# Performance work log

Measured on AMD Instinct MI355X. Metric: run time of the kernel, lower is better.

Reference implementation:

```python
import jax, jax.numpy as jnp
import numpy as np

N_NODES = 262144
N_EDGES = 524288
EMB = 256
HID = 256
NODE_VOC = 50000
POS_VOC = 1000
LN_EPS = 1e-5


def layer_norm(x, g, b):
    m = jnp.mean(x, axis=-1, keepdims=True)
    v = jnp.var(x, axis=-1, keepdims=True)
    return (x - m) * jax.lax.rsqrt(v + LN_EPS) * g + b


def sage_conv(x, src, dst, Wl, bl, Wr):
    # PyG SAGEConv, aggr='add': out = lin_l(sum_{j in N(i)} x_j) + lin_r(x_i)
    agg = jax.ops.segment_sum(x[src], dst, num_segments=N_NODES)  # [N, d_in]
    return agg @ Wl.T + bl + x @ Wr.T


def setup_inputs() -> dict:
    key = jax.random.key(0)
    ks = jax.random.split(key, 16)
    s = 0.02
    node_emb = jax.random.randint(ks[0], (N_NODES,), 0, NODE_VOC)
    pos = jax.random.randint(ks[1], (N_NODES,), 0, POS_VOC)
    edge = jax.random.randint(ks[2], (2, N_EDGES), 0, N_NODES)
    node_tab = jax.random.normal(ks[3], (NODE_VOC, EMB), jnp.float32) * s
    pos_tab = jax.random.normal(ks[4], (POS_VOC, EMB), jnp.float32) * s
    pos_tab = pos_tab.at[0].set(0.0)  # padding_idx=0
    g_emb = jnp.ones((EMB,), jnp.float32)
    b_emb = jnp.zeros((EMB,), jnp.float32)
    Wl0 = jax.random.normal(ks[5], (HID, EMB), jnp.float32) * s
    bl0 = jnp.zeros((HID,), jnp.float32)
    Wr0 = jax.random.normal(ks[6], (HID, EMB), jnp.float32) * s
    g0 = jnp.ones((HID,), jnp.float32)
    b0 = jnp.zeros((HID,), jnp.float32)
    Wl1 = jax.random.normal(ks[7], (EMB, HID), jnp.float32) * s
    bl1 = jnp.zeros((EMB,), jnp.float32)
    Wr1 = jax.random.normal(ks[8], (EMB, HID), jnp.float32) * s
    g1 = jnp.ones((EMB,), jnp.float32)
    b1 = jnp.zeros((EMB,), jnp.float32)
    return {"node_emb": node_emb, "pos": pos, "edge": edge,
            "node_tab": node_tab, "pos_tab": pos_tab,
            "g_emb": g_emb, "b_emb": b_emb,
            "Wl0": Wl0, "bl0": bl0, "Wr0": Wr0, "g0": g0, "b0": b0,
            "Wl1": Wl1, "bl1": bl1, "Wr1": Wr1, "g1": g1, "b1": b1}


def reference(node_emb, pos, edge, node_tab, pos_tab, g_emb, b_emb,
              Wl0, bl0, Wr0, g0, b0, Wl1, bl1, Wr1, g1, b1):
    src, dst = edge[0], edge[1]
    # embed + scale + positional emb; dropout is identity in eval
    h = node_tab[node_emb] * jnp.sqrt(jnp.float32(EMB)) + pos_tab[pos]
    h = layer_norm(h, g_emb, b_emb)
    for (Wl, bl, Wr, g, b) in ((Wl0, bl0, Wr0, g0, b0), (Wl1, bl1, Wr1, g1, b1)):
        h_ = jax.nn.relu(sage_conv(h, src, dst, Wl, bl, Wr))
        h = layer_norm(h_ + h, g, b)
    return h
```

## Files before the change

kernel.cpp:

```cpp
#include <hip/hip_runtime.h>
#include <hip/hip_bf16.h>
#include <stdint.h>

#define N_NODES 262144
#define N_EDGES 524288
#define EMB 256
#define LN_EPS 1e-5f
#define CSR_CAP 1024

typedef unsigned short u16;
typedef unsigned int u32;
typedef __bf16 bf16_t;
typedef __bf16 bf16x8 __attribute__((ext_vector_type(8)));
typedef float f32x4 __attribute__((ext_vector_type(4)));

__device__ __forceinline__ u16 f2bf(float f) {
    u32 u = __float_as_uint(f);
    u32 r = u + 0x7fffu + ((u >> 16) & 1u);
    return (u16)(r >> 16);
}
__device__ __forceinline__ float bf2f(u16 b) { return __uint_as_float(((u32)b) << 16); }
__device__ __forceinline__ float lo16(u32 x) { return __uint_as_float(x << 16); }
__device__ __forceinline__ float hi16(u32 x) { return __uint_as_float(x & 0xffff0000u); }

__device__ __forceinline__ void async_copy16(void* lds, const void* g) {
    __builtin_amdgcn_global_load_lds(
        (const __attribute__((address_space(1))) u32*)g,
        (__attribute__((address_space(3))) u32*)lds, 16, 0, 0);
}

__global__ __launch_bounds__(256) void convert_w_kernel(
    const float* __restrict__ a, const float* __restrict__ b,
    const float* __restrict__ c, const float* __restrict__ d,
    u16* __restrict__ out)
{
    int seg = blockIdx.x >> 6;
    int blk = blockIdx.x & 63;
    const float* src = (seg == 0) ? a : (seg == 1) ? b : (seg == 2) ? c : d;
    int off = blk * 1024 + threadIdx.x * 4;
    float4 v = *(const float4*)(src + off);
    uint2 o;
    o.x = (u32)f2bf(v.x) | ((u32)f2bf(v.y) << 16);
    o.y = (u32)f2bf(v.z) | ((u32)f2bf(v.w) << 16);
    *(uint2*)(out + seg * 65536 + off) = o;
}

__global__ __launch_bounds__(256) void embed_ln_kernel(
    const int* __restrict__ node_emb, const int* __restrict__ pos,
    const float* __restrict__ node_tab, const float* __restrict__ pos_tab,
    const float* __restrict__ g_emb, const float* __restrict__ b_emb,
    u16* __restrict__ h0)
{
    const int wid = threadIdx.x >> 6, lane = threadIdx.x & 63;
    const int row = blockIdx.x * 4 + wid;
    const int idx = node_emb[row];
    const int p = pos[row];
    float4 ra = *(const float4*)(node_tab + (size_t)idx * EMB + lane * 4);
    float4 rb = *(const float4*)(pos_tab + (size_t)p * EMB + lane * 4);
    float v0 = ra.x * 16.f + rb.x;
    float v1 = ra.y * 16.f + rb.y;
    float v2 = ra.z * 16.f + rb.z;
    float v3 = ra.w * 16.f + rb.w;
    float s = v0 + v1 + v2 + v3;
    float sq = v0 * v0 + v1 * v1 + v2 * v2 + v3 * v3;
    #pragma unroll
    for (int m = 1; m < 64; m <<= 1) { s += __shfl_xor(s, m); sq += __shfl_xor(sq, m); }
    float mean = s * (1.f / 256.f);
    float var = sq * (1.f / 256.f) - mean * mean;
    float rstd = rsqrtf(var + LN_EPS);
    float4 rg = *(const float4*)(g_emb + lane * 4);
    float4 rbt = *(const float4*)(b_emb + lane * 4);
    float o0 = (v0 - mean) * rstd * rg.x + rbt.x;
    float o1 = (v1 - mean) * rstd * rg.y + rbt.y;
    float o2 = (v2 - mean) * rstd * rg.z + rbt.z;
    float o3 = (v3 - mean) * rstd * rg.w + rbt.w;
    uint2 out;
    out.x = (u32)f2bf(o0) | ((u32)f2bf(o1) << 16);
    out.y = (u32)f2bf(o2) | ((u32)f2bf(o3) << 16);
    *(uint2*)(h0 + (size_t)row * EMB + lane * 4) = out;
}

__global__ __launch_bounds__(256) void hist_kernel(const int* __restrict__ dst, int* __restrict__ deg) {
    int e = blockIdx.x * 256 + threadIdx.x;
    atomicAdd(&deg[dst[e]], 1);
}

__global__ __launch_bounds__(1024) void scan1_kernel(const int* __restrict__ deg,
                                                     int* __restrict__ incl, int* __restrict__ bsum) {
    __shared__ int tmp[1024];
    int t = threadIdx.x, g = blockIdx.x * 1024 + t;
    tmp[t] = deg[g];
    __syncthreads();
    for (int off = 1; off < 1024; off <<= 1) {
        int x = (t >= off) ? tmp[t - off] : 0;
        __syncthreads();
        tmp[t] += x;
        __syncthreads();
    }
    incl[g] = tmp[t];
    if (t == 1023) bsum[blockIdx.x] = tmp[t];
}

__global__ __launch_bounds__(256) void scan2_kernel(const int* __restrict__ bsum, int* __restrict__ boff) {
    __shared__ int tmp[256];
    int t = threadIdx.x;
    int own = bsum[t];
    tmp[t] = own;
    __syncthreads();
    for (int off = 1; off < 256; off <<= 1) {
        int x = (t >= off) ? tmp[t - off] : 0;
        __syncthreads();
        tmp[t] += x;
        __syncthreads();
    }
    boff[t] = tmp[t] - own;
}

__global__ __launch_bounds__(256) void scan3_kernel(const int* __restrict__ incl, const int* __restrict__ deg,
                                                    const int* __restrict__ boff,
                                                    int* __restrict__ rowstart, int* __restrict__ cursor) {
    int g = blockIdx.x * 256 + threadIdx.x;
    int v = incl[g] - deg[g] + boff[g >> 10];
    rowstart[g] = v;
    cursor[g] = v;
    if (g == N_NODES - 1) rowstart[N_NODES] = N_EDGES;
}

__global__ __launch_bounds__(256) void scatter_kernel(const int* __restrict__ src, const int* __restrict__ dst,
                                                      int* __restrict__ cursor, int* __restrict__ csr) {
    int e = blockIdx.x * 256 + threadIdx.x;
    int slot = atomicAdd(&cursor[dst[e]], 1);
    csr[slot] = src[e];
}

template<bool F32OUT>
__global__ __launch_bounds__(512, 4) void gemm_fused_kernel(
    const u16* __restrict__ Hin,
    const int* __restrict__ rowstart, const int* __restrict__ csr,
    const u16* __restrict__ Wl, const u16* __restrict__ Wr,
    const float* __restrict__ bias, const float* __restrict__ gam, const float* __restrict__ bet,
    u16* __restrict__ outb, float* __restrict__ outf)
{
    __shared__ alignas(16) u16 aggA[4 * 64 * 64];
    __shared__ alignas(16) u16 lB[256 * 64];
    __shared__ int ls_row[72];
    __shared__ int lcsr[CSR_CAP];
    __shared__ float s_sum[64];
    __shared__ float s_sq[64];

    const int tid = threadIdx.x;
    const int wid = tid >> 6, lane = tid & 63;
    const int quad = lane >> 4, l16 = lane & 15;
    const int wrow = wid >> 2, wcol = wid & 3;
    const int m0 = blockIdx.x * 64;
    const int lsrc = ((lane & 7) ^ (lane >> 3)) * 8;

    auto stageB = [&](int s) {
        const int k0 = s * 64;
        const u16* Bsrc = (k0 < 256) ? (Wl + k0) : (Wr + (k0 - 256));
        #pragma unroll
        for (int t = 0; t < 4; ++t) {
            int q = wid * 4 + t;
            int n = q * 8 + (lane >> 3);
            async_copy16((char*)lB + q * 1024, Bsrc + (size_t)n * EMB + lsrc);
        }
    };
    auto stageH = [&](int t) {
        int row = tid >> 3;
        int kg = (tid & 7) ^ (row & 7);
        async_copy16((char*)aggA + (t - 4) * 8192 + tid * 16,
                     Hin + (size_t)(m0 + row) * EMB + (t - 4) * 64 + kg * 8);
    };

    stageB(0);

    const int beg_all = rowstart[m0];
    const int end_all = rowstart[m0 + 64];
    const int cnt = end_all - beg_all;
    if (tid < 65) ls_row[tid] = rowstart[m0 + tid];
    const int lim = (cnt < CSR_CAP) ? cnt : CSR_CAP;
    for (int e = tid; e < lim; e += 512) lcsr[e] = csr[beg_all + e];
    asm volatile("s_waitcnt lgkmcnt(0)\n\ts_barrier" ::: "memory");

    {
        const int grp = tid >> 4, gl = tid & 15;
        #pragma unroll 1
        for (int i = 0; i < 2; ++i) {
            const int r = grp * 2 + i;
            const int beg = ls_row[r];
            const int end = ls_row[r + 1];
            float a0[16] = {}, a1[16] = {};
            int j = beg;
            for (; j + 1 < end; j += 2) {
                int sl0 = j - beg_all, sl1 = sl0 + 1;
                int s0 = (sl0 < CSR_CAP) ? lcsr[sl0] : csr[j];
                int s1 = (sl1 < CSR_CAP) ? lcsr[sl1] : csr[j + 1];
                const u16* p0 = Hin + (size_t)s0 * EMB + gl * 16;
                const u16* p1 = Hin + (size_t)s1 * EMB + gl * 16;
                uint4 q0 = *(const uint4*)p0, q2 = *(const uint4*)(p0 + 8);
                uint4 q1 = *(const uint4*)p1, q3 = *(const uint4*)(p1 + 8);
                a0[0]  += lo16(q0.x); a0[1]  += hi16(q0.x);
                a0[2]  += lo16(q0.y); a0[3]  += hi16(q0.y);
                a0[4]  += lo16(q0.z); a0[5]  += hi16(q0.z);
                a0[6]  += lo16(q0.w); a0[7]  += hi16(q0.w);
                a0[8]  += lo16(q2.x); a0[9]  += hi16(q2.x);
                a0[10] += lo16(q2.y); a0[11] += hi16(q2.y);
                a0[12] += lo16(q2.z); a0[13] += hi16(q2.z);
                a0[14] += lo16(q2.w); a0[15] += hi16(q2.w);
                a1[0]  += lo16(q1.x); a1[1]  += hi16(q1.x);
                a1[2]  += lo16(q1.y); a1[3]  += hi16(q1.y);
                a1[4]  += lo16(q1.z); a1[5]  += hi16(q1.z);
                a1[6]  += lo16(q1.w); a1[7]  += hi16(q1.w);
                a1[8]  += lo16(q3.x); a1[9]  += hi16(q3.x);
                a1[10] += lo16(q3.y); a1[11] += hi16(q3.y);
                a1[12] += lo16(q3.z); a1[13] += hi16(q3.z);
                a1[14] += lo16(q3.w); a1[15] += hi16(q3.w);
            }
            if (j < end) {
                int sl0 = j - beg_all;
                int s0 = (sl0 < CSR_CAP) ? lcsr[sl0] : csr[j];
                const u16* p0 = Hin + (size_t)s0 * EMB + gl * 16;
                uint4 q0 = *(const uint4*)p0, q2 = *(const uint4*)(p0 + 8);
                a0[0]  += lo16(q0.x); a0[1]  += hi16(q0.x);
                a0[2]  += lo16(q0.y); a0[3]  += hi16(q0.y);
                a0[4]  += lo16(q0.z); a0[5]  += hi16(q0.z);
                a0[6]  += lo16(q0.w); a0[7]  += hi16(q0.w);
                a0[8]  += lo16(q2.x); a0[9]  += hi16(q2.x);
                a0[10] += lo16(q2.y); a0[11] += hi16(q2.y);
                a0[12] += lo16(q2.z); a0[13] += hi16(q2.z);
                a0[14] += lo16(q2.w); a0[15] += hi16(q2.w);
            }
            uint4 o0, o1;
            o0.x = (u32)f2bf(a0[0]  + a1[0])  | ((u32)f2bf(a0[1]  + a1[1])  << 16);
            o0.y = (u32)f2bf(a0[2]  + a1[2])  | ((u32)f2bf(a0[3]  + a1[3])  << 16);
            o0.z = (u32)f2bf(a0[4]  + a1[4])  | ((u32)f2bf(a0[5]  + a1[5])  << 16);
            o0.w = (u32)f2bf(a0[6]  + a1[6])  | ((u32)f2bf(a0[7]  + a1[7])  << 16);
            o1.x = (u32)f2bf(a0[8]  + a1[8])  | ((u32)f2bf(a0[9]  + a1[9])  << 16);
            o1.y = (u32)f2bf(a0[10] + a1[10]) | ((u32)f2bf(a0[11] + a1[11]) << 16);
            o1.z = (u32)f2bf(a0[12] + a1[12]) | ((u32)f2bf(a0[13] + a1[13]) << 16);
            o1.w = (u32)f2bf(a0[14] + a1[14]) | ((u32)f2bf(a0[15] + a1[15]) << 16);
            int kg0 = (2 * gl) & 7;
            int cg0 = kg0 ^ (r & 7);
            int cg1 = (kg0 + 1) ^ (r & 7);
            u16* base = &aggA[(gl >> 2) * 4096 + r * 64];
            *(uint4*)(base + cg0 * 8) = o0;
            *(uint4*)(base + cg1 * 8) = o1;
        }
    }
    asm volatile("s_waitcnt lgkmcnt(0)\n\ts_barrier" ::: "memory");

    f32x4 acc[2][4] = {};
    #pragma unroll
    for (int s = 0; s < 8; ++s) {
        if (s > 0) stageB(s);
        if (s >= 1 && s <= 4) stageH(s + 3);
        if (s >= 1 && s <= 4) asm volatile("s_waitcnt vmcnt(1)\n\ts_barrier" ::: "memory");
        else                  asm volatile("s_waitcnt vmcnt(0)\n\ts_barrier" ::: "memory");

        const u16* la = aggA + (s & 3) * 4096;
        #pragma unroll
        for (int kk = 0; kk < 2; ++kk) {
            const int g = (((kk * 4 + quad) ^ (l16 & 7)) * 8);
            bf16x8 af[2], bfr[4];
            #pragma unroll
            for (int mt = 0; mt < 2; ++mt)
                af[mt] = *(const bf16x8*)&la[(wrow * 32 + mt * 16 + l16) * 64 + g];
            #pragma unroll
            for (int nt = 0; nt < 4; ++nt)
                bfr[nt] = *(const bf16x8*)&lB[(wcol * 64 + nt * 16 + l16) * 64 + g];
            #pragma unroll
            for (int mt = 0; mt < 2; ++mt)
                #pragma unroll
                for (int nt = 0; nt < 4; ++nt)
                    acc[mt][nt] = __builtin_amdgcn_mfma_f32_16x16x32_bf16(af[mt], bfr[nt], acc[mt][nt], 0, 0, 0);
        }
        asm volatile("s_waitcnt lgkmcnt(0)\n\ts_barrier" ::: "memory");
    }

    if (tid < 64) { s_sum[tid] = 0.f; s_sq[tid] = 0.f; }
    __syncthreads();

    const int cb = wcol * 64;
    float blv[4], gv[4], bv[4];
    #pragma unroll
    for (int nt = 0; nt < 4; ++nt) {
        int col = cb + nt * 16 + l16;
        blv[nt] = bias[col]; gv[nt] = gam[col]; bv[nt] = bet[col];
    }

    #pragma unroll
    for (int mt = 0; mt < 2; ++mt) {
        #pragma unroll
        for (int i = 0; i < 4; ++i) {
            int r = wrow * 32 + mt * 16 + quad * 4 + i;
            int rowg = m0 + r;
            float rs = 0.f, rq = 0.f;
            #pragma unroll
            for (int nt = 0; nt < 4; ++nt) {
                int col = cb + nt * 16 + l16;
                float v = acc[mt][nt][i] + blv[nt];
                v = fmaxf(v, 0.f);
                v += bf2f(Hin[(size_t)rowg * EMB + col]);
                acc[mt][nt][i] = v;
                rs += v; rq += v * v;
            }
            #pragma unroll
            for (int m = 1; m < 16; m <<= 1) { rs += __shfl_xor(rs, m); rq += __shfl_xor(rq, m); }
            if (l16 == 0) { atomicAdd(&s_sum[r], rs); atomicAdd(&s_sq[r], rq); }
        }
    }
    __syncthreads();

    #pragma unroll
    for (int mt = 0; mt < 2; ++mt) {
        #pragma unroll
        for (int i = 0; i < 4; ++i) {
            int r = wrow * 32 + mt * 16 + quad * 4 + i;
            int rowg = m0 + r;
            float mean = s_sum[r] * (1.f / 256.f);
            float var = s_sq[r] * (1.f / 256.f) - mean * mean;
            float rstd = rsqrtf(var + LN_EPS);
            #pragma unroll
            for (int nt = 0; nt < 4; ++nt) {
                int col = cb + nt * 16 + l16;
                float o = (acc[mt][nt][i] - mean) * rstd * gv[nt] + bv[nt];
                if (F32OUT) outf[(size_t)rowg * EMB + col] = o;
                else        outb[(size_t)rowg * EMB + col] = f2bf(o);
            }
        }
    }
}

extern "C" void kernel_launch(void* const* d_in, const int* in_sizes, int n_in,
                              void* d_out, int out_size, void* d_ws, size_t ws_size,
                              hipStream_t stream)
{
    const int* node_emb = (const int*)d_in[0];
    const int* pos      = (const int*)d_in[1];
    const int* edge     = (const int*)d_in[2];
    const float* node_tab = (const float*)d_in[3];
    const float* pos_tab  = (const float*)d_in[4];
    const float* g_emb    = (const float*)d_in[5];
    const float* b_emb    = (const float*)d_in[6];
    const float* Wl0 = (const float*)d_in[7];
    const float* bl0 = (const float*)d_in[8];
    const float* Wr0 = (const float*)d_in[9];
    const float* g0  = (const float*)d_in[10];
    const float* b0  = (const float*)d_in[11];
    const float* Wl1 = (const float*)d_in[12];
    const float* bl1 = (const float*)d_in[13];
    const float* Wr1 = (const float*)d_in[14];
    const float* g1  = (const float*)d_in[15];
    const float* b1  = (const float*)d_in[16];

    char* w = (char*)d_ws;
    auto alloc = [&](size_t bytes) { char* p = w; w += (bytes + 255) & ~(size_t)255; return p; };
    u16* h0       = (u16*)alloc((size_t)N_NODES * EMB * 2);
    u16* h1       = (u16*)alloc((size_t)N_NODES * EMB * 2);
    u16* wbf      = (u16*)alloc((size_t)4 * 65536 * 2);
    int* deg      = (int*)alloc((size_t)N_NODES * 4);
    int* incl     = (int*)alloc((size_t)N_NODES * 4);
    int* rowstart = (int*)alloc((size_t)(N_NODES + 1) * 4);
    int* cursor   = (int*)alloc((size_t)N_NODES * 4);
    int* csr      = (int*)alloc((size_t)N_EDGES * 4);
    int* bsum     = (int*)alloc(256 * 4);
    int* boff     = (int*)alloc(256 * 4);

    float* outf = (float*)d_out;

    const int* srcv = edge;
    const int* dstv = edge + N_EDGES;

    hipMemsetAsync(deg, 0, (size_t)N_NODES * 4, stream);
    convert_w_kernel<<<256, 256, 0, stream>>>(Wl0, Wr0, Wl1, Wr1, wbf);
    embed_ln_kernel<<<N_NODES / 4, 256, 0, stream>>>(node_emb, pos, node_tab, pos_tab, g_emb, b_emb, h0);
    hist_kernel<<<N_EDGES / 256, 256, 0, stream>>>(dstv, deg);
    scan1_kernel<<<N_NODES / 1024, 1024, 0, stream>>>(deg, incl, bsum);
    scan2_kernel<<<1, 256, 0, stream>>>(bsum, boff);
    scan3_kernel<<<N_NODES / 256, 256, 0, stream>>>(incl, deg, boff, rowstart, cursor);
    scatter_kernel<<<N_EDGES / 256, 256, 0, stream>>>(srcv, dstv, cursor, csr);

    gemm_fused_kernel<false><<<N_NODES / 64, 512, 0, stream>>>(
        h0, rowstart, csr, wbf, wbf + 65536, bl0, g0, b0, h1, nullptr);
    gemm_fused_kernel<true><<<N_NODES / 64, 512, 0, stream>>>(
        h1, rowstart, csr, wbf + 131072, wbf + 196608, bl1, g1, b1, nullptr, outf);
}
```

Measured before the change: 810.2 us.

## Stage weights through registers and reuse LDS-resident H tiles for residual

Weight tiles are now loaded one stage ahead into registers and written to LDS at the start of each stage, replacing async global-to-LDS copies. The node's own feature rows are staged into a new LDS buffer plus reused aggA slots, so the residual add in the epilogue reads from LDS instead of re-reading the rows from global memory. This removes redundant global reads in the epilogue and changes the pipeline schedule. It costs extra registers and 8 KB more LDS, which may reduce occupancy.

After: 778.5 us. -3.9%, faster.

```diff
diff --git a/kernel.cpp b/kernel.cpp
--- a/kernel.cpp
+++ b/kernel.cpp
@@ -142,6 +142,7 @@
     u16* __restrict__ outb, float* __restrict__ outf)
 {
     __shared__ alignas(16) u16 aggA[4 * 64 * 64];
+    __shared__ alignas(16) u16 hX[64 * 64];
     __shared__ alignas(16) u16 lB[256 * 64];
     __shared__ int ls_row[72];
     __shared__ int lcsr[CSR_CAP];
@@ -155,24 +156,34 @@
     const int m0 = blockIdx.x * 64;
     const int lsrc = ((lane & 7) ^ (lane >> 3)) * 8;
 
-    auto stageB = [&](int s) {
+    uint4 breg0, breg1, breg2, breg3;
+    auto loadB = [&](int s) {
         const int k0 = s * 64;
         const u16* Bsrc = (k0 < 256) ? (Wl + k0) : (Wr + (k0 - 256));
-        #pragma unroll
-        for (int t = 0; t < 4; ++t) {
-            int q = wid * 4 + t;
-            int n = q * 8 + (lane >> 3);
-            async_copy16((char*)lB + q * 1024, Bsrc + (size_t)n * EMB + lsrc);
-        }
+        const int n0 = (wid * 4 + 0) * 8 + (lane >> 3);
+        const int n1 = (wid * 4 + 1) * 8 + (lane >> 3);
+        const int n2 = (wid * 4 + 2) * 8 + (lane >> 3);
+        const int n3 = (wid * 4 + 3) * 8 + (lane >> 3);
+        breg0 = *(const uint4*)(Bsrc + (size_t)n0 * EMB + lsrc);
+        breg1 = *(const uint4*)(Bsrc + (size_t)n1 * EMB + lsrc);
+        breg2 = *(const uint4*)(Bsrc + (size_t)n2 * EMB + lsrc);
+        breg3 = *(const uint4*)(Bsrc + (size_t)n3 * EMB + lsrc);
     };
-    auto stageH = [&](int t) {
+    auto writeB = [&]() {
+        *(uint4*)((char*)lB + (wid * 4 + 0) * 1024 + lane * 16) = breg0;
+        *(uint4*)((char*)lB + (wid * 4 + 1) * 1024 + lane * 16) = breg1;
+        *(uint4*)((char*)lB + (wid * 4 + 2) * 1024 + lane * 16) = breg2;
+        *(uint4*)((char*)lB + (wid * 4 + 3) * 1024 + lane * 16) = breg3;
+    };
+    auto stageH = [&](int t, u16* dst) {
         int row = tid >> 3;
         int kg = (tid & 7) ^ (row & 7);
-        async_copy16((char*)aggA + (t - 4) * 8192 + tid * 16,
+        async_copy16((char*)dst + tid * 16,
                      Hin + (size_t)(m0 + row) * EMB + (t - 4) * 64 + kg * 8);
     };
 
-    stageB(0);
+    loadB(0);
+    stageH(4, hX);
 
     const int beg_all = rowstart[m0];
     const int end_all = rowstart[m0 + 64];
@@ -192,9 +203,9 @@
             float a0[16] = {}, a1[16] = {};
             int j = beg;
             for (; j + 1 < end; j += 2) {
-                int sl0 = j - beg_all, sl1 = sl0 + 1;
-                int s0 = (sl0 < CSR_CAP) ? lcsr[sl0] : csr[j];
-                int s1 = (sl1 < CSR_CAP) ? lcsr[sl1] : csr[j + 1];
+                int sl = j - beg_all;
+                int s0 = (sl < CSR_CAP) ? lcsr[sl] : csr[j];
+                int s1 = (sl + 1 < CSR_CAP) ? lcsr[sl + 1] : csr[j + 1];
                 const u16* p0 = Hin + (size_t)s0 * EMB + gl * 16;
                 const u16* p1 = Hin + (size_t)s1 * EMB + gl * 16;
                 uint4 q0 = *(const uint4*)p0, q2 = *(const uint4*)(p0 + 8);
@@ -217,8 +228,8 @@
                 a1[14] += lo16(q3.w); a1[15] += hi16(q3.w);
             }
             if (j < end) {
-                int sl0 = j - beg_all;
-                int s0 = (sl0 < CSR_CAP) ? lcsr[sl0] : csr[j];
+                int sl = j - beg_all;
+                int s0 = (sl < CSR_CAP) ? lcsr[sl] : csr[j];
                 const u16* p0 = Hin + (size_t)s0 * EMB + gl * 16;
                 uint4 q0 = *(const uint4*)p0, q2 = *(const uint4*)(p0 + 8);
                 a0[0]  += lo16(q0.x); a0[1]  += hi16(q0.x);
@@ -252,12 +263,14 @@
     f32x4 acc[2][4] = {};
     #pragma unroll
     for (int s = 0; s < 8; ++s) {
-        if (s > 0) stageB(s);
-        if (s >= 1 && s <= 4) stageH(s + 3);
-        if (s >= 1 && s <= 4) asm volatile("s_waitcnt vmcnt(1)\n\ts_barrier" ::: "memory");
-        else                  asm volatile("s_waitcnt vmcnt(0)\n\ts_barrier" ::: "memory");
-
-        const u16* la = aggA + (s & 3) * 4096;
+        if (s >= 1 && s <= 3) stageH(s + 4, aggA + (s - 1) * 4096);
+        writeB();
+        if (s < 7) loadB(s + 1);
+        asm volatile("s_waitcnt lgkmcnt(0)\n\ts_barrier" ::: "memory");
+
+        const u16* la = (s < 4) ? (aggA + s * 4096)
+                      : (s == 4) ? hX
+                                 : (aggA + (s - 5) * 4096);
         #pragma unroll
         for (int kk = 0; kk < 2; ++kk) {
             const int g = (((kk * 4 + quad) ^ (l16 & 7)) * 8);
@@ -280,6 +293,7 @@
     if (tid < 64) { s_sum[tid] = 0.f; s_sq[tid] = 0.f; }
     __syncthreads();
 
+    const u16* resbuf = (wcol == 0) ? hX : (aggA + (wcol - 1) * 4096);
     const int cb = wcol * 64;
     float blv[4], gv[4], bv[4];
     #pragma unroll
@@ -293,14 +307,14 @@
         #pragma unroll
         for (int i = 0; i < 4; ++i) {
             int r = wrow * 32 + mt * 16 + quad * 4 + i;
-            int rowg = m0 + r;
             float rs = 0.f, rq = 0.f;
             #pragma unroll
             for (int nt = 0; nt < 4; ++nt) {
-                int col = cb + nt * 16 + l16;
+                int cc = nt * 16 + l16;
+                float res = bf2f(resbuf[r * 64 + (((cc >> 3) ^ (r & 7)) << 3) + (cc & 7)]);
                 float v = acc[mt][nt][i] + blv[nt];
                 v = fmaxf(v, 0.f);
-                v += bf2f(Hin[(size_t)rowg * EMB + col]);
+                v += res;
                 acc[mt][nt][i] = v;
                 rs += v; rq += v * v;
             }
```
